# Performance work log

Measured on AMD Instinct MI355X. Metric: run time of the kernel, lower is better.

Reference implementation:

```python
import jax, jax.numpy as jnp
import numpy as np

B, T, HID = 2, 2048, 1536
H, HKV, D = 12, 2, 128
EPS = 1e-6
NEG = -1e9


def setup_inputs() -> dict:
    key = jax.random.key(0)
    ks = jax.random.split(key, 8)
    # rotary embeddings built from real angles (cos/sin of position*inv_freq)
    inv_freq = 1.0 / (10000.0 ** (jnp.arange(0, D, 2, dtype=jnp.float32) / D))  # [D/2]
    pos = jnp.arange(T, dtype=jnp.float32)
    ang = pos[:, None] * inv_freq[None, :]                       # [T, D/2]
    emb = jnp.concatenate([ang, ang], axis=-1)                   # [T, D]
    cos = jnp.broadcast_to(jnp.cos(emb)[None], (B, T, D))
    sin = jnp.broadcast_to(jnp.sin(emb)[None], (B, T, D))
    # additive causal mask [1,1,T,T]
    causal = jnp.tril(jnp.ones((T, T), dtype=bool))
    attention_mask = jnp.where(causal, 0.0, NEG).astype(jnp.float32)[None, None]
    s = 0.02
    return {
        "hidden_states": jax.random.normal(ks[0], (B, T, HID), jnp.float32),
        "cos": cos,
        "sin": sin,
        "attention_mask": attention_mask,
        "q_w": jax.random.normal(ks[1], (H * D, HID), jnp.float32) * s,
        "k_w": jax.random.normal(ks[2], (HKV * D, HID), jnp.float32) * s,
        "v_w": jax.random.normal(ks[3], (HKV * D, HID), jnp.float32) * s,
        "o_w": jax.random.normal(ks[4], (HID, H * D), jnp.float32) * s,
        "q_norm_w": jnp.ones((D,), jnp.float32),
        "k_norm_w": jnp.ones((D,), jnp.float32),
    }


def _rms_norm(x, w):
    # per-head RMSNorm over last dim (head_dim), computed in fp32
    xf = x.astype(jnp.float32)
    var = jnp.mean(xf * xf, axis=-1, keepdims=True)
    return (w * (xf * jax.lax.rsqrt(var + EPS))).astype(x.dtype)


def _rotate_half(x):
    x1, x2 = jnp.split(x, 2, axis=-1)
    return jnp.concatenate([-x2, x1], axis=-1)


def reference(hidden_states, cos, sin, attention_mask, q_w, k_w, v_w, o_w, q_norm_w, k_norm_w):
    b, t, _ = hidden_states.shape
    n_rep = H // HKV
    scale = D ** -0.5

    # projections -> [B, n_heads, T, D]
    q = (hidden_states @ q_w.T).reshape(b, t, H, D)
    k = (hidden_states @ k_w.T).reshape(b, t, HKV, D)
    v = (hidden_states @ v_w.T).reshape(b, t, HKV, D).transpose(0, 2, 1, 3)

    # per-head QK RMSNorm, then to [B, H, T, D]
    q = _rms_norm(q, q_norm_w).transpose(0, 2, 1, 3)
    k = _rms_norm(k, k_norm_w).transpose(0, 2, 1, 3)

    # RoPE (cos/sin broadcast over head axis)
    c = cos[:, None, :, :]
    s = sin[:, None, :, :]
    q = q * c + _rotate_half(q) * s
    k = k * c + _rotate_half(k) * s

    # GQA repeat_kv: [B, HKV, T, D] -> [B, H, T, D]
    k = jnp.repeat(k, n_rep, axis=1)
    v = jnp.repeat(v, n_rep, axis=1)

    attn = jnp.einsum('bhqd,bhkd->bhqk', q, k) * scale + attention_mask
    attn = jax.nn.softmax(attn.astype(jnp.float32), axis=-1).astype(q.dtype)
    out = jnp.einsum('bhqk,bhkd->bhqd', attn, v)
    out = out.transpose(0, 2, 1, 3).reshape(b, t, H * D)
    return out @ o_w.T
```

## Files before the change

### kernel.cpp

```cpp
#include <hip/hip_runtime.h>
#include <hip/hip_bf16.h>


#define B_   2
#define T_   2048
#define HID_ 1536
#define H_   12
#define HKV_ 2
#define D_   128
#define GQ_  (H_ / HKV_)
#define NQKV_ 2048
#define LOG2E_ 1.4426950408889634f
#define SCALE2_ (0.08838834764831845f * LOG2E_)

typedef unsigned short u16;
typedef __attribute__((ext_vector_type(4))) float f32x4;
typedef __attribute__((ext_vector_type(8))) short bf16x8;
typedef __attribute__((ext_vector_type(4))) unsigned short u16x4;
typedef __attribute__((ext_vector_type(8))) unsigned short u16x8;

__device__ __forceinline__ u16 f2b(float f) {
  union { __hip_bfloat16 h; u16 u; } cv;
  cv.h = __float2bfloat16(f);
  return cv.u;
}
__device__ __forceinline__ float b2f(u16 u) {
  union { float f; unsigned i; } cv;
  cv.i = ((unsigned)u) << 16;
  return cv.f;
}

__device__ __forceinline__ void glds16(const u16* g, u16* l) {
  __builtin_amdgcn_global_load_lds((const __attribute__((address_space(1))) void*)g,
                                   (__attribute__((address_space(3))) void*)l, 16, 0, 0);
}

__global__ __launch_bounds__(256) void cvt_f32_bf16(const float* __restrict__ src,
                                                    u16* __restrict__ dst, int n4) {
  int i = blockIdx.x * 256 + threadIdx.x;
  const int stride = gridDim.x * 256;
  for (; i < n4; i += stride) {
    const float4 v = reinterpret_cast<const float4*>(src)[i];
    u16x4 o = {f2b(v.x), f2b(v.y), f2b(v.z), f2b(v.w)};
    reinterpret_cast<u16x4*>(dst)[i] = o;
  }
}

#define NQ4_ 589824
#define NK4_ 98304
__global__ __launch_bounds__(256) void cvt_wqkv(const float* __restrict__ q_w,
                                                const float* __restrict__ k_w,
                                                const float* __restrict__ v_w,
                                                u16* __restrict__ qkvw) {
  int i = blockIdx.x * 256 + threadIdx.x;
  const int stride = gridDim.x * 256;
  const int total = NQ4_ + 2 * NK4_;
  for (; i < total; i += stride) {
    float4 v;
    if (i < NQ4_) v = reinterpret_cast<const float4*>(q_w)[i];
    else if (i < NQ4_ + NK4_) v = reinterpret_cast<const float4*>(k_w)[i - NQ4_];
    else v = reinterpret_cast<const float4*>(v_w)[i - NQ4_ - NK4_];
    u16x4 o = {f2b(v.x), f2b(v.y), f2b(v.z), f2b(v.w)};
    reinterpret_cast<u16x4*>(qkvw)[i] = o;
  }
}

__global__ __launch_bounds__(256) void gemm_bt(const u16* __restrict__ A,
                                               const u16* __restrict__ W,
                                               float* __restrict__ C,
                                               int M, int N, int K) {
  __shared__ __align__(16) u16 As[128 * 64];
  __shared__ __align__(16) u16 Ws[128 * 64];
  const int tid  = threadIdx.x;
  const int lane = tid & 63;
  const int wid  = tid >> 6;
  const int wr = wid >> 1, wc = wid & 1;
  const int l15 = lane & 15, kg = lane >> 4;
  const int rowBase = blockIdx.y * 128;
  const int colBase = blockIdx.x * 128;

  const int srow = lane >> 3;
  const int scol = (lane & 7) << 3;
  const u16* Ab = A + (size_t)(rowBase + wid * 32 + srow) * K + scol;
  const u16* Wb = W + (size_t)(colBase + wid * 32 + srow) * K + scol;

  const f32x4 zero4 = {0.f, 0.f, 0.f, 0.f};
  f32x4 acc[4][4];
#pragma unroll
  for (int m = 0; m < 4; ++m)
#pragma unroll
    for (int n = 0; n < 4; ++n) acc[m][n] = zero4;

  for (int k0 = 0; k0 < K; k0 += 64) {
    __syncthreads();
#pragma unroll
    for (int c = 0; c < 4; ++c) {
      glds16(Ab + (size_t)(c * 8) * K + k0, &As[(wid * 4 + c) * 512]);
      glds16(Wb + (size_t)(c * 8) * K + k0, &Ws[(wid * 4 + c) * 512]);
    }
    __syncthreads();
    bf16x8 a[4][2], b[4][2];
#pragma unroll
    for (int m = 0; m < 4; ++m)
#pragma unroll
      for (int ks = 0; ks < 2; ++ks)
        a[m][ks] = *reinterpret_cast<const bf16x8*>(
            &As[(wr * 64 + m * 16 + l15) * 64 + ks * 32 + kg * 8]);
#pragma unroll
    for (int n = 0; n < 4; ++n)
#pragma unroll
      for (int ks = 0; ks < 2; ++ks)
        b[n][ks] = *reinterpret_cast<const bf16x8*>(
            &Ws[(wc * 64 + n * 16 + l15) * 64 + ks * 32 + kg * 8]);
#pragma unroll
    for (int m = 0; m < 4; ++m)
#pragma unroll
      for (int n = 0; n < 4; ++n)
#pragma unroll
        for (int ks = 0; ks < 2; ++ks)
          acc[m][n] = __builtin_amdgcn_mfma_f32_16x16x32_bf16(a[m][ks], b[n][ks],
                                                              acc[m][n], 0, 0, 0);
  }
#pragma unroll
  for (int m = 0; m < 4; ++m) {
    const int row0 = rowBase + wr * 64 + m * 16 + kg * 4;
#pragma unroll
    for (int n = 0; n < 4; ++n) {
      const int col = colBase + wc * 64 + n * 16 + l15;
#pragma unroll
      for (int r = 0; r < 4; ++r) C[(size_t)(row0 + r) * N + col] = acc[m][n][r];
    }
  }
}

__global__ __launch_bounds__(256) void gemm_qkv(
    const u16* __restrict__ A, const u16* __restrict__ W,
    const float* __restrict__ cosb, const float* __restrict__ sinb,
    const float* __restrict__ q_nw, const float* __restrict__ k_nw,
    u16* __restrict__ q_b, u16* __restrict__ k_b, u16* __restrict__ vt_b) {
  __shared__ __align__(16) u16 smem[128 * 137];
  u16* As = smem;
  u16* Ws = smem + 8192;
  const int tid  = threadIdx.x;
  const int lane = tid & 63;
  const int wid  = tid >> 6;
  const int wr = wid >> 1, wc = wid & 1;
  const int l15 = lane & 15, kg = lane >> 4;
  const int rowBase = blockIdx.y * 128;
  const int colBase = blockIdx.x * 128;
  const int K = HID_;

  const int srow = lane >> 3;
  const int scol = (lane & 7) << 3;
  const u16* Ab = A + (size_t)(rowBase + wid * 32 + srow) * K + scol;
  const u16* Wb = W + (size_t)(colBase + wid * 32 + srow) * K + scol;

  const f32x4 zero4 = {0.f, 0.f, 0.f, 0.f};
  f32x4 acc[4][4];
#pragma unroll
  for (int m = 0; m < 4; ++m)
#pragma unroll
    for (int n = 0; n < 4; ++n) acc[m][n] = zero4;

  for (int k0 = 0; k0 < K; k0 += 64) {
    __syncthreads();
#pragma unroll
    for (int c = 0; c < 4; ++c) {
      glds16(Ab + (size_t)(c * 8) * K + k0, &As[(wid * 4 + c) * 512]);
      glds16(Wb + (size_t)(c * 8) * K + k0, &Ws[(wid * 4 + c) * 512]);
    }
    __syncthreads();
    bf16x8 a[4][2], b[4][2];
#pragma unroll
    for (int m = 0; m < 4; ++m)
#pragma unroll
      for (int ks = 0; ks < 2; ++ks)
        a[m][ks] = *reinterpret_cast<const bf16x8*>(
            &As[(wr * 64 + m * 16 + l15) * 64 + ks * 32 + kg * 8]);
#pragma unroll
    for (int n = 0; n < 4; ++n)
#pragma unroll
      for (int ks = 0; ks < 2; ++ks)
        b[n][ks] = *reinterpret_cast<const bf16x8*>(
            &Ws[(wc * 64 + n * 16 + l15) * 64 + ks * 32 + kg * 8]);
#pragma unroll
    for (int m = 0; m < 4; ++m)
#pragma unroll
      for (int n = 0; n < 4; ++n)
#pragma unroll
        for (int ks = 0; ks < 2; ++ks)
          acc[m][n] = __builtin_amdgcn_mfma_f32_16x16x32_bf16(a[m][ks], b[n][ks],
                                                              acc[m][n], 0, 0, 0);
  }

  __syncthreads();
#pragma unroll
  for (int m = 0; m < 4; ++m)
#pragma unroll
    for (int n = 0; n < 4; ++n)
#pragma unroll
      for (int r = 0; r < 4; ++r)
        smem[(wr * 64 + m * 16 + kg * 4 + r) * 137 + wc * 64 + n * 16 + l15] =
            f2b(acc[m][n][r]);
  __syncthreads();

  const int ct = blockIdx.x;
  const int b = rowBase >> 11;
  if (ct < 14) {
    const float* nw = (ct < 12) ? q_nw : k_nw;
    const float nwl = nw[lane], nwh = nw[lane + 64];
    const float sc = (ct < 12) ? SCALE2_ : 1.0f;
    u16* dstbase = (ct < 12) ? (q_b + (size_t)(b * H_ + ct) * T_ * D_)
                             : (k_b + (size_t)(b * HKV_ + (ct - 12)) * T_ * D_);
    for (int i = 0; i < 32; ++i) {
      const int row = wid * 32 + i;
      const int tok = rowBase + row;
      const int t = tok & (T_ - 1);
      const float x1 = b2f(smem[row * 137 + lane]);
      const float x2 = b2f(smem[row * 137 + lane + 64]);
      float ss = x1 * x1 + x2 * x2;
#pragma unroll
      for (int msk = 32; msk >= 1; msk >>= 1) ss += __shfl_xor(ss, msk);
      const float rinv = rsqrtf(ss * (1.0f / D_) + 1e-6f);
      const float c1 = cosb[(size_t)tok * D_ + lane];
      const float c2 = cosb[(size_t)tok * D_ + lane + 64];
      const float s1 = sinb[(size_t)tok * D_ + lane];
      const float s2 = sinb[(size_t)tok * D_ + lane + 64];
      const float n1 = x1 * rinv * nwl, n2 = x2 * rinv * nwh;
      u16* dst = dstbase + (size_t)t * D_;
      dst[lane] = f2b((n1 * c1 - n2 * s1) * sc);
      dst[lane + 64] = f2b((n2 * c2 + n1 * s2) * sc);
    }
  } else {
    const int hv = ct - 14;
    const int tp = (lane & 32) | (((lane >> 2) & 3) << 3) | (((lane >> 4) & 1) << 2) |
                   (lane & 3);
    u16* vb = vt_b + (size_t)(b * HKV_ + hv) * D_ * T_;
    const int tb = rowBase & (T_ - 1);
    for (int it = 0; it < 64; ++it) {
      const int d = wid * 32 + (it >> 1), half = it & 1;
      const float x = b2f(smem[(half * 64 + lane) * 137 + d]);
      vb[(size_t)d * T_ + tb + half * 64 + tp] = f2b(x);
    }
  }
}

__constant__ int QT_ARR[40] = {15,15,15,15,14,14,11,11,11,10, 7, 7, 3,
                               14,14,13,13,13,13,12,12,10,10, 9, 9, 6, 6,
                               12,12, 9, 8, 8, 8, 5, 5, 2,
                                4, 4, 1, 0};
__constant__ int C_ARR[40]  = { 0, 1, 2, 3, 0, 1, 0, 1, 2, 0, 0, 1,-1,
                                2, 3, 0, 1, 2, 3, 0, 1, 1, 2, 0, 1, 0, 1,
                                2, 3, 2, 0, 1, 2, 0, 1,-1,
                                0, 1,-1,-1};
__device__ __forceinline__ int nc_of(int qt) { return (qt < 8) ? 2 : ((qt < 12) ? 3 : 4); }
__device__ __forceinline__ int mlbase_of(int qt) {
  return (qt < 8) ? 2 * (qt - 4) : ((qt < 12) ? 8 + 3 * (qt - 8) : 20 + 4 * (qt - 12));
}
__device__ __forceinline__ int pbase_of(int qt) {
  return (qt < 8) ? (qt - 4) : ((qt < 12) ? 4 + 2 * (qt - 8) : 12 + 3 * (qt - 12));
}

__global__ __launch_bounds__(256) void attn_kernel(const u16* __restrict__ q_b,
                                                   const u16* __restrict__ k_b,
                                                   const u16* __restrict__ vt_b,
                                                   u16* __restrict__ aout,
                                                   u16* __restrict__ po0,
                                                   float2* __restrict__ ml) {
  __shared__ __align__(16) u16 Ks[64 * 128];
  __shared__ __align__(16) u16 Vs[128 * 64];
  const int id = blockIdx.x;
  const int item = id / 24;
  const int bh = id - item * 24;
  const int qt = QT_ARR[item];
  const int c = C_ARR[item];
  int kt0, ktend;
  bool partial;
  if (c < 0) {
    kt0 = 0; ktend = 2 * qt + 1; partial = false;
  } else {
    const int nt = 2 * qt + 2;
    const int nc = nc_of(qt);
    const int base = nt / nc, rem = nt - base * nc;
    kt0 = c * base + (c < rem ? c : rem);
    ktend = kt0 + base + (c < rem ? 1 : 0) - 1;
    partial = true;
  }
  const int b = bh / H_, h = bh - b * H_;
  const int kvh = h / GQ_;
  const int tid = threadIdx.x;
  const int w = tid >> 6, lane = tid & 63;
  const int l15 = lane & 15, kg = lane >> 4;
  const int qbase = qt * 128;

  const u16* Kb = k_b + (size_t)(b * HKV_ + kvh) * T_ * D_;
  const u16* Vb = vt_b + (size_t)(b * HKV_ + kvh) * D_ * T_;

  bf16x8 qf[2][4];
#pragma unroll
  for (int qb = 0; qb < 2; ++qb) {
    const u16* qrow =
        q_b + ((size_t)(b * H_ + h) * T_ + qbase + w * 32 + qb * 16 + l15) * D_;
#pragma unroll
    for (int s4 = 0; s4 < 4; ++s4)
      qf[qb][s4] = *reinterpret_cast<const bf16x8*>(qrow + s4 * 32 + kg * 8);
  }

  int kK[4], vK[4];
#pragma unroll
  for (int cc = 0; cc < 4; ++cc) {
    const int ch = w * 4 + cc;
    const int kr = ch * 4 + (lane >> 4);
    kK[cc] = kr * D_ + (((lane & 15) << 3) ^ ((kr & 7) << 3));
    const int dr = ch * 8 + (lane >> 3);
    vK[cc] = dr * T_ + (((lane & 7) << 3) ^ ((dr & 7) << 3));
  }
  const int xorv = (l15 & 7) << 3;

  const f32x4 zero4 = {0.f, 0.f, 0.f, 0.f};
  f32x4 o[2][8];
#pragma unroll
  for (int qb = 0; qb < 2; ++qb)
#pragma unroll
    for (int n = 0; n < 8; ++n) o[qb][n] = zero4;
  float m[2] = {0.f, 0.f};
  float lsum[2] = {0.f, 0.f};

  for (int kt = kt0; kt <= ktend; ++kt) {
    __syncthreads();
    {
      const size_t kb = (size_t)kt * 64;
#pragma unroll
      for (int cc = 0; cc < 4; ++cc) {
        glds16(Kb + kb * D_ + kK[cc], &Ks[(w * 4 + cc) * 512]);
        glds16(Vb + kb + vK[cc], &Vs[(w * 4 + cc) * 512]);
      }
    }
    __syncthreads();
    f32x4 sc[2][4];
#pragma unroll
    for (int qb = 0; qb < 2; ++qb)
#pragma unroll
      for (int n = 0; n < 4; ++n) sc[qb][n] = zero4;
    __builtin_amdgcn_s_setprio(1);
#pragma unroll
    for (int n = 0; n < 4; ++n)
#pragma unroll
      for (int s4 = 0; s4 < 4; ++s4) {
        const int koff = (n * 16 + l15) * 128 + ((s4 * 32 + kg * 8) ^ xorv);
        bf16x8 kf = *reinterpret_cast<const bf16x8*>(&Ks[koff]);
#pragma unroll
        for (int qb = 0; qb < 2; ++qb)
          sc[qb][n] = __builtin_amdgcn_mfma_f32_16x16x32_bf16(kf, qf[qb][s4],
                                                              sc[qb][n], 0, 0, 0);
      }
    __builtin_amdgcn_s_setprio(0);
    if (kt >= 2 * qt) {
#pragma unroll
      for (int qb = 0; qb < 2; ++qb) {
        const int qg = w * 32 + qb * 16 + l15;
        const int kbb = (kt - 2 * qt) * 64;
#pragma unroll
        for (int n = 0; n < 4; ++n)
#pragma unroll
          for (int r = 0; r < 4; ++r)
            if (kbb + n * 16 + kg * 4 + r > qg) sc[qb][n][r] = -3e38f;
      }
    }
    float pm[2];
#pragma unroll
    for (int qb = 0; qb < 2; ++qb) {
      float v = sc[qb][0][0];
#pragma unroll
      for (int n = 0; n < 4; ++n)
#pragma unroll
        for (int r = 0; r < 4; ++r) v = fmaxf(v, sc[qb][n][r]);
      v = fmaxf(v, __shfl_xor(v, 16));
      v = fmaxf(v, __shfl_xor(v, 32));
      pm[qb] = v;
    }
    if (__any((pm[0] > m[0] + 8.f) | (pm[1] > m[1] + 8.f))) {
#pragma unroll
      for (int qb = 0; qb < 2; ++qb) {
        const float mn = fmaxf(m[qb], pm[qb]);
        const float al = exp2f(m[qb] - mn);
        m[qb] = mn;
        lsum[qb] *= al;
        float alT[4];
#pragma unroll
        for (int r = 0; r < 4; ++r)
          alT[r] = __shfl(al, (lane & 48) | (kg * 4 + r));
#pragma unroll
        for (int n = 0; n < 8; ++n)
#pragma unroll
          for (int r = 0; r < 4; ++r) o[qb][n][r] *= alT[r];
      }
    }
#pragma unroll
    for (int qb = 0; qb < 2; ++qb) {
      float rs = 0.f;
#pragma unroll
      for (int n = 0; n < 4; ++n)
#pragma unroll
        for (int r = 0; r < 4; ++r) {
          const float p = exp2f(sc[qb][n][r] - m[qb]);
          sc[qb][n][r] = p;
          rs += p;
        }
      rs += __shfl_xor(rs, 16);
      rs += __shfl_xor(rs, 32);
      lsum[qb] += rs;
    }
    bf16x8 pf[2][2];
#pragma unroll
    for (int qb = 0; qb < 2; ++qb)
#pragma unroll
      for (int ks = 0; ks < 2; ++ks)
#pragma unroll
        for (int r = 0; r < 4; ++r) {
          pf[qb][ks][r] = (short)f2b(sc[qb][2 * ks][r]);
          pf[qb][ks][r + 4] = (short)f2b(sc[qb][2 * ks + 1][r]);
        }
    __builtin_amdgcn_s_setprio(1);
#pragma unroll
    for (int n = 0; n < 8; ++n)
#pragma unroll
      for (int ks = 0; ks < 2; ++ks) {
        const int voff = (n * 16 + l15) * 64 + ((ks * 32 + kg * 8) ^ xorv);
        bf16x8 vf = *reinterpret_cast<const bf16x8*>(&Vs[voff]);
#pragma unroll
        for (int qb = 0; qb < 2; ++qb)
          o[qb][n] = __builtin_amdgcn_mfma_f32_16x16x32_bf16(pf[qb][ks], vf,
                                                             o[qb][n], 0, 0, 0);
      }
    __builtin_amdgcn_s_setprio(0);
  }

  if (!partial) {
    float invT[2][4];
#pragma unroll
    for (int qb = 0; qb < 2; ++qb) {
      const float inv = 1.0f / lsum[qb];
#pragma unroll
      for (int r = 0; r < 4; ++r)
        invT[qb][r] = __shfl(inv, (lane & 48) | (kg * 4 + r));
    }
#pragma unroll
    for (int qb = 0; qb < 2; ++qb) {
      const int t0 = qbase + w * 32 + qb * 16 + kg * 4;
#pragma unroll
      for (int n = 0; n < 8; ++n)
#pragma unroll
        for (int r = 0; r < 4; ++r)
          aout[(size_t)(b * T_ + t0 + r) * (H_ * D_) + h * D_ + n * 16 + l15] =
              f2b(o[qb][n][r] * invT[qb][r]);
    }
  } else {
    const int mlslot = bh * 36 + mlbase_of(qt) + c;
    if (kg == 0) {
#pragma unroll
      for (int qb = 0; qb < 2; ++qb) {
        float2 v;
        v.x = m[qb];
        v.y = lsum[qb];
        ml[(size_t)mlslot * 128 + w * 32 + qb * 16 + l15] = v;
      }
    }
    if (c == 0) {
#pragma unroll
      for (int qb = 0; qb < 2; ++qb) {
        const int t0 = qbase + w * 32 + qb * 16 + kg * 4;
#pragma unroll
        for (int n = 0; n < 8; ++n)
#pragma unroll
          for (int r = 0; r < 4; ++r)
            aout[(size_t)(b * T_ + t0 + r) * (H_ * D_) + h * D_ + n * 16 + l15] =
                f2b(o[qb][n][r]);
      }
    } else {
      const int pslot = bh * 24 + pbase_of(qt) + (c - 1);
#pragma unroll
      for (int qb = 0; qb < 2; ++qb) {
        const int row0 = w * 32 + qb * 16 + kg * 4;
#pragma unroll
        for (int n = 0; n < 8; ++n)
#pragma unroll
          for (int r = 0; r < 4; ++r)
            po0[((size_t)pslot * 128 + row0 + r) * 128 + n * 16 + l15] =
                f2b(o[qb][n][r]);
      }
    }
  }
}

__global__ __launch_bounds__(256) void combine_kernel(u16* __restrict__ aout,
                                                      const u16* __restrict__ po0,
                                                      const float2* __restrict__ ml) {
  const int qt = 4 + blockIdx.x;
  const int bh = blockIdx.y;
  const int nc = nc_of(qt);
  const int mlb = bh * 36 + mlbase_of(qt);
  const int pb = bh * 24 + pbase_of(qt);
  const int b = bh / H_, h = bh - b * H_;
  const int t0 = qt * 128;
  const int tid = threadIdx.x;
  const int row = tid >> 1;
  const int colc = (tid & 1) << 6;

  float ms[4], ls[4];
  float mm = -3e38f;
  for (int cc = 0; cc < nc; ++cc) {
    const float2 v = ml[(size_t)(mlb + cc) * 128 + row];
    ms[cc] = v.x; ls[cc] = v.y;
    mm = fmaxf(mm, v.x);
  }
  float lt = 0.f;
  float scl[4];
  for (int cc = 0; cc < nc; ++cc) {
    scl[cc] = exp2f(ms[cc] - mm);
    lt += ls[cc] * scl[cc];
  }
  const float inv = 1.0f / lt;
  for (int cc = 0; cc < nc; ++cc) scl[cc] *= inv;

  u16* a = aout + (size_t)(b * T_ + t0 + row) * (H_ * D_) + h * D_ + colc;
#pragma unroll
  for (int j = 0; j < 8; ++j) {
    u16x8 v0 = *reinterpret_cast<const u16x8*>(a + j * 8);
    float acc[8];
#pragma unroll
    for (int e = 0; e < 8; ++e) acc[e] = b2f(v0[e]) * scl[0];
    for (int cc = 1; cc < nc; ++cc) {
      const u16* p = po0 + ((size_t)(pb + cc - 1) * 128 + row) * 128 + colc;
      u16x8 vc = *reinterpret_cast<const u16x8*>(p + j * 8);
#pragma unroll
      for (int e = 0; e < 8; ++e) acc[e] += b2f(vc[e]) * scl[cc];
    }
    u16x8 outv;
#pragma unroll
    for (int e = 0; e < 8; ++e) outv[e] = f2b(acc[e]);
    *reinterpret_cast<u16x8*>(a + j * 8) = outv;
  }
}

extern "C" void kernel_launch(void* const* d_in, const int* in_sizes, int n_in,
                              void* d_out, int out_size, void* d_ws, size_t ws_size,
                              hipStream_t stream) {
  const float* hidden = (const float*)d_in[0];
  const float* cosb   = (const float*)d_in[1];
  const float* sinb   = (const float*)d_in[2];
  const float* q_w  = (const float*)d_in[4];
  const float* k_w  = (const float*)d_in[5];
  const float* v_w  = (const float*)d_in[6];
  const float* o_w  = (const float*)d_in[7];
  const float* q_nw = (const float*)d_in[8];
  const float* k_nw = (const float*)d_in[9];
  float* out = (float*)d_out;

  char* ws = (char*)d_ws;
  const size_t MB = 1u << 20;
  u16*    hidden_b = (u16*)(ws);
  u16*    qkvw     = (u16*)(ws + 12 * MB);
  u16*    q_b      = (u16*)(ws + 18 * MB);
  u16*    k_b      = (u16*)(ws + 30 * MB);
  u16*    vt_b     = (u16*)(ws + 32 * MB);
  u16*    aout     = (u16*)(ws);
  u16*    owb      = (u16*)(ws + 12 * MB);
  float2* ml       = (float2*)(ws + 17 * MB);
  u16*    po0      = (u16*)d_out;

  const dim3 blk(256);
  const int M = B_ * T_;

  cvt_f32_bf16<<<2048, blk, 0, stream>>>(hidden, hidden_b, (B_ * T_ * HID_) / 4);
  cvt_wqkv<<<3072, blk, 0, stream>>>(q_w, k_w, v_w, qkvw);

  gemm_qkv<<<dim3(NQKV_ / 128, M / 128), blk, 0, stream>>>(
      hidden_b, qkvw, cosb, sinb, q_nw, k_nw, q_b, k_b, vt_b);

  cvt_f32_bf16<<<2048, blk, 0, stream>>>(o_w, owb, (H_ * D_ * HID_) / 4);

  attn_kernel<<<960, blk, 0, stream>>>(q_b, k_b, vt_b, aout, po0, ml);
  combine_kernel<<<dim3(12, B_ * H_), blk, 0, stream>>>(aout, po0, ml);

  gemm_bt<<<dim3(HID_ / 128, M / 128), blk, 0, stream>>>(aout, owb, out,
                                                         M, HID_, HID_);
}
```

Measured before the change: 203.1 us.

## Double-buffer K/V tiles in attention and switch softmax to natural exp

The attention loop now keeps two shared-memory K/V buffers and issues the global-to-LDS loads for the next key tile before computing on the current one. It waits with explicit vmcnt counts and raw barriers instead of two __syncthreads per tile. This is meant to hide global load latency behind the MFMA work. Separately, the log2e factor is removed from the Q scaling and exp2f is replaced with __expf. That change is numerically equivalent in intent but adds a multiply inside __expf, and the doubled LDS use may lower occupancy.

```diff
diff --git a/kernel.cpp b/kernel.cpp
--- a/kernel.cpp
+++ b/kernel.cpp
@@ -10,8 +10,7 @@
 #define D_   128
 #define GQ_  (H_ / HKV_)
 #define NQKV_ 2048
-#define LOG2E_ 1.4426950408889634f
-#define SCALE2_ (0.08838834764831845f * LOG2E_)
+#define SCALE_ 0.08838834764831845f
 
 typedef unsigned short u16;
 typedef __attribute__((ext_vector_type(4))) float f32x4;
@@ -209,7 +208,7 @@
   if (ct < 14) {
     const float* nw = (ct < 12) ? q_nw : k_nw;
     const float nwl = nw[lane], nwh = nw[lane + 64];
-    const float sc = (ct < 12) ? SCALE2_ : 1.0f;
+    const float sc = (ct < 12) ? SCALE_ : 1.0f;
     u16* dstbase = (ct < 12) ? (q_b + (size_t)(b * H_ + ct) * T_ * D_)
                              : (k_b + (size_t)(b * HKV_ + (ct - 12)) * T_ * D_);
     for (int i = 0; i < 32; ++i) {
@@ -267,8 +266,8 @@
                                                    u16* __restrict__ aout,
                                                    u16* __restrict__ po0,
                                                    float2* __restrict__ ml) {
-  __shared__ __align__(16) u16 Ks[64 * 128];
-  __shared__ __align__(16) u16 Vs[128 * 64];
+  __shared__ __align__(16) u16 Ks[2][64 * 128];
+  __shared__ __align__(16) u16 Vs[2][128 * 64];
   const int id = blockIdx.x;
   const int item = id / 24;
   const int bh = id - item * 24;
@@ -326,17 +325,33 @@
   float m[2] = {0.f, 0.f};
   float lsum[2] = {0.f, 0.f};
 
+  {
+    const size_t kb = (size_t)kt0 * 64;
+#pragma unroll
+    for (int cc = 0; cc < 4; ++cc) {
+      glds16(Kb + kb * D_ + kK[cc], &Ks[0][(w * 4 + cc) * 512]);
+      glds16(Vb + kb + vK[cc], &Vs[0][(w * 4 + cc) * 512]);
+    }
+  }
+  int cur = 0;
+
   for (int kt = kt0; kt <= ktend; ++kt) {
-    __syncthreads();
-    {
-      const size_t kb = (size_t)kt * 64;
+    if (kt < ktend) {
+      const size_t kb = (size_t)(kt + 1) * 64;
 #pragma unroll
       for (int cc = 0; cc < 4; ++cc) {
-        glds16(Kb + kb * D_ + kK[cc], &Ks[(w * 4 + cc) * 512]);
-        glds16(Vb + kb + vK[cc], &Vs[(w * 4 + cc) * 512]);
-      }
-    }
-    __syncthreads();
+        glds16(Kb + kb * D_ + kK[cc], &Ks[cur ^ 1][(w * 4 + cc) * 512]);
+        glds16(Vb + kb + vK[cc], &Vs[cur ^ 1][(w * 4 + cc) * 512]);
+      }
+      asm volatile("s_waitcnt vmcnt(8)" ::: "memory");
+    } else {
+      asm volatile("s_waitcnt vmcnt(0)" ::: "memory");
+    }
+    __builtin_amdgcn_s_barrier();
+    asm volatile("" ::: "memory");
+
+    const u16* Kc = &Ks[cur][0];
+    const u16* Vc = &Vs[cur][0];
     f32x4 sc[2][4];
 #pragma unroll
     for (int qb = 0; qb < 2; ++qb)
@@ -348,7 +363,7 @@
 #pragma unroll
       for (int s4 = 0; s4 < 4; ++s4) {
         const int koff = (n * 16 + l15) * 128 + ((s4 * 32 + kg * 8) ^ xorv);
-        bf16x8 kf = *reinterpret_cast<const bf16x8*>(&Ks[koff]);
+        bf16x8 kf = *reinterpret_cast<const bf16x8*>(&Kc[koff]);
 #pragma unroll
         for (int qb = 0; qb < 2; ++qb)
           sc[qb][n] = __builtin_amdgcn_mfma_f32_16x16x32_bf16(kf, qf[qb][s4],
@@ -383,7 +398,7 @@
 #pragma unroll
       for (int qb = 0; qb < 2; ++qb) {
         const float mn = fmaxf(m[qb], pm[qb]);
-        const float al = exp2f(m[qb] - mn);
+        const float al = __expf(m[qb] - mn);
         m[qb] = mn;
         lsum[qb] *= al;
         float alT[4];
@@ -403,7 +418,7 @@
       for (int n = 0; n < 4; ++n)
 #pragma unroll
         for (int r = 0; r < 4; ++r) {
-          const float p = exp2f(sc[qb][n][r] - m[qb]);
+          const float p = __expf(sc[qb][n][r] - m[qb]);
           sc[qb][n][r] = p;
           rs += p;
         }
@@ -427,13 +442,15 @@
 #pragma unroll
       for (int ks = 0; ks < 2; ++ks) {
         const int voff = (n * 16 + l15) * 64 + ((ks * 32 + kg * 8) ^ xorv);
-        bf16x8 vf = *reinterpret_cast<const bf16x8*>(&Vs[voff]);
+        bf16x8 vf = *reinterpret_cast<const bf16x8*>(&Vc[voff]);
 #pragma unroll
         for (int qb = 0; qb < 2; ++qb)
           o[qb][n] = __builtin_amdgcn_mfma_f32_16x16x32_bf16(pf[qb][ks], vf,
                                                              o[qb][n], 0, 0, 0);
       }
     __builtin_amdgcn_s_setprio(0);
+    __builtin_amdgcn_s_barrier();
+    cur ^= 1;
   }
 
   if (!partial) {
@@ -517,7 +534,7 @@
   float lt = 0.f;
   float scl[4];
   for (int cc = 0; cc < nc; ++cc) {
-    scl[cc] = exp2f(ms[cc] - mm);
+    scl[cc] = __expf(ms[cc] - mm);
     lt += ls[cc] * scl[cc];
   }
   const float inv = 1.0f / lt;
```

Result: no change. 202.1 us (-0.5%).
